# Kernel optimization log

Hardware: AMD Instinct MI355X
Metric: run time of the kernel (lower is better)

Reference implementation:

```python
import jax, jax.numpy as jnp
import numpy as np

S, B, L, V, D, T, G = 16, 8, 8, 32000, 1024, 512, 3


def setup_inputs() -> dict:
    key = jax.random.key(0)
    k = jax.random.split(key, 10)
    s = 0.05
    return {
        "encoded_hidden": jax.random.normal(k[0], (B, D), jnp.float32),
        "encoded_outputs": jax.random.normal(k[1], (B, T, D), jnp.float32),
        "story": jax.random.randint(k[2], (B, T), 0, V),
        "trg_batches": jax.random.randint(k[3], (B, S, L), 0, V),
        "embedding": jax.random.normal(k[4], (V, D), jnp.float32) * 0.1,
        "w_ih": jax.random.normal(k[5], (3 * D, D), jnp.float32) * s,
        "w_hh": jax.random.normal(k[6], (3 * D, D), jnp.float32) * s,
        "b_ih": jnp.zeros((3 * D,), jnp.float32),
        "b_hh": jnp.zeros((3 * D,), jnp.float32),
        "w_ratio_w": jax.random.normal(k[7], (1, 3 * D), jnp.float32) * s,
        "w_ratio_b": jnp.zeros((1,), jnp.float32),
        "w_gate_w": jax.random.normal(k[8], (G, D), jnp.float32) * s,
        "w_gate_b": jnp.zeros((G,), jnp.float32),
        "slot_emb": jax.random.normal(k[9], (S, D), jnp.float32) * 0.1,
    }


def reference(encoded_hidden, encoded_outputs, story, trg_batches, embedding,
              w_ih, w_hh, b_ih, b_hh, w_ratio_w, w_ratio_b,
              w_gate_w, w_gate_b, slot_emb):
    # Decoder inputs per (slot, step): step 0 = slot embedding,
    # step i>0 = embedding of teacher-forced target token i-1.  -> x: (S,L,B,D)
    x0 = jnp.broadcast_to(slot_emb[:, None, None, :], (S, 1, B, D))
    xt = jnp.transpose(embedding[trg_batches[:, :, :L - 1]], (1, 2, 0, 3))  # (S,L-1,B,D)
    x = jnp.concatenate([x0, xt], axis=1)

    # Single GRU step; hidden is reset to the encoder hidden each step (as in source),
    # so decoder_state == new hidden and all (slot,step) cells are independent.
    h0 = encoded_hidden  # (B,D)
    gi = jnp.einsum('slbd,ed->slbe', x, w_ih) + b_ih          # (S,L,B,3D)
    gh = h0 @ w_hh.T + b_hh                                    # (B,3D)
    ir, iz, inn = jnp.split(gi, 3, axis=-1)
    hr, hz, hn = jnp.split(gh, 3, axis=-1)
    r = jax.nn.sigmoid(ir + hr)
    z = jax.nn.sigmoid(iz + hz)
    n = jnp.tanh(inn + r * hn)
    h = (1.0 - z) * n + z * h0                                 # (S,L,B,D)

    # History attention; NOTE: context uses the RAW scores (source quirk).
    scores = jnp.einsum('slbd,btd->slbt', h, encoded_outputs)  # (S,L,B,T)
    probs = jax.nn.softmax(scores, axis=-1)
    context = jnp.einsum('slbt,btd->slbd', scores, encoded_outputs)

    # Vocab distribution p_vocab = softmax(h @ E^T)
    p_vocab = jax.nn.softmax(jnp.einsum('slbd,vd->slbv', h, embedding), axis=-1)

    # Pointer-generator gate
    feat = jnp.concatenate([h, context, x], axis=-1)           # (S,L,B,3D)
    p_gen = jax.nn.sigmoid(jnp.einsum('slbe,oe->slbo', feat, w_ratio_w) + w_ratio_b)  # (S,L,B,1)

    # Copy distribution via scatter-add of attention probs onto vocab ids
    def scatter_one(p_b, story_b):  # p_b: (S,L,T), story_b: (T,)
        return jnp.zeros((S, L, V), p_b.dtype).at[:, :, story_b].add(p_b)
    p_ctx = jax.vmap(scatter_one, in_axes=(2, 0), out_axes=2)(probs, story)  # (S,L,B,V)

    p_final = p_gen * p_vocab + (1.0 - p_gen) * p_ctx
    ptr_outputs = jnp.transpose(p_final, (0, 2, 1, 3))         # (S,B,L,V)
    gate_outputs = context[:, 0] @ w_gate_w.T + w_gate_b       # (S,B,G), from step 0
    return ptr_outputs, gate_outputs
```

## Files before the change

### kernel.cpp

```cpp
#include <hip/hip_runtime.h>

#define S_ 16
#define B_ 8
#define L_ 8
#define V_ 32000
#define D_ 1024
#define T_ 512
#define G_ 3
#define M_ 1024
#define E3_ 3072
#define NT_ 250

typedef unsigned short U16;
typedef __attribute__((ext_vector_type(8))) short short8;
typedef __attribute__((ext_vector_type(4))) float f32x4;

__device__ __forceinline__ U16 f2bf(float f) {
  union { float f; unsigned u; } c; c.f = f;
  unsigned u = c.u;
  return (U16)((u + 0x7FFFu + ((u >> 16) & 1u)) >> 16);
}
__device__ __forceinline__ float bf2f(U16 h) {
  union { unsigned u; float f; } c; c.u = ((unsigned)h) << 16;
  return c.f;
}
__device__ __forceinline__ void split2(float f, U16& hi, U16& lo) {
  hi = f2bf(f);
  lo = f2bf(f - bf2f(hi));
}

__global__ void k_cast_emb(const float* __restrict__ emb, U16* __restrict__ emb_bf) {
  int idx = blockIdx.x * 256 + threadIdx.x;
  float4 v = ((const float4*)emb)[idx];
  ushort4 o;
  o.x = f2bf(v.x); o.y = f2bf(v.y); o.z = f2bf(v.z); o.w = f2bf(v.w);
  ((ushort4*)emb_bf)[idx] = o;
}

__global__ void k_cast_wih(const float* __restrict__ w, U16* __restrict__ wh, U16* __restrict__ wl) {
  int idx = blockIdx.x * 256 + threadIdx.x;
  float4 v = ((const float4*)w)[idx];
  ushort4 h4, l4;
  split2(v.x, h4.x, l4.x); split2(v.y, h4.y, l4.y);
  split2(v.z, h4.z, l4.z); split2(v.w, h4.w, l4.w);
  ((ushort4*)wh)[idx] = h4;
  ((ushort4*)wl)[idx] = l4;
}

__global__ void k_cast_enc(const float* __restrict__ enc,
                           U16* __restrict__ enc_h, U16* __restrict__ enc_l,
                           U16* __restrict__ encT_h, U16* __restrict__ encT_l) {
  __shared__ U16 hs[32][36];
  __shared__ U16 ls[32][36];
  int b = blockIdx.z, t0 = blockIdx.x * 32, d0 = blockIdx.y * 32;
  int r  = threadIdx.x >> 3;
  int c4 = (threadIdx.x & 7) * 4;
  size_t src_idx = ((size_t)(b * T_ + t0 + r)) * D_ + d0 + c4;
  float4 v = *(const float4*)(enc + src_idx);
  ushort4 h4, l4;
  split2(v.x, h4.x, l4.x); split2(v.y, h4.y, l4.y);
  split2(v.z, h4.z, l4.z); split2(v.w, h4.w, l4.w);
  *(ushort4*)(enc_h + src_idx) = h4;
  *(ushort4*)(enc_l + src_idx) = l4;
  hs[r][c4+0] = h4.x; hs[r][c4+1] = h4.y; hs[r][c4+2] = h4.z; hs[r][c4+3] = h4.w;
  ls[r][c4+0] = l4.x; ls[r][c4+1] = l4.y; ls[r][c4+2] = l4.z; ls[r][c4+3] = l4.w;
  __syncthreads();
  ushort4 th, tl;
  th.x = hs[c4+0][r]; th.y = hs[c4+1][r]; th.z = hs[c4+2][r]; th.w = hs[c4+3][r];
  tl.x = ls[c4+0][r]; tl.y = ls[c4+1][r]; tl.z = ls[c4+2][r]; tl.w = ls[c4+3][r];
  size_t dst_idx = ((size_t)(b * D_ + d0 + r)) * T_ + t0 + c4;
  *(ushort4*)(encT_h + dst_idx) = th;
  *(ushort4*)(encT_l + dst_idx) = tl;
}

__global__ void k_build_x(const float* __restrict__ emb, const float* __restrict__ slot_emb,
                          const int* __restrict__ trg, float* __restrict__ x,
                          U16* __restrict__ x_h, U16* __restrict__ x_l) {
  int m = blockIdx.x;
  int d = threadIdx.x * 4;
  int b = m >> 7, s = (m >> 3) & 15, l = m & 7;
  const float* src;
  if (l == 0) src = slot_emb + s * D_;
  else        src = emb + (size_t)trg[b * (S_ * L_) + s * L_ + (l - 1)] * D_;
  float4 v = *(const float4*)(src + d);
  *(float4*)(x + (size_t)m * D_ + d) = v;
  ushort4 h4, l4;
  split2(v.x, h4.x, l4.x); split2(v.y, h4.y, l4.y);
  split2(v.z, h4.z, l4.z); split2(v.w, h4.w, l4.w);
  *(ushort4*)(x_h + (size_t)m * D_ + d) = h4;
  *(ushort4*)(x_l + (size_t)m * D_ + d) = l4;
}

__global__ void k_gh(const float* __restrict__ h0, const float* __restrict__ w_hh,
                     const float* __restrict__ b_hh, float* __restrict__ gh) {
  int b = blockIdx.y;
  int e = blockIdx.x * 64 + (threadIdx.x >> 2);
  int part = threadIdx.x & 3;
  const float* hr = h0 + b * D_ + part * 256;
  const float* wr = w_hh + (size_t)e * D_ + part * 256;
  float s = 0.f;
  for (int i = 0; i < 256; ++i) s += hr[i] * wr[i];
  s += __shfl_xor(s, 1);
  s += __shfl_xor(s, 2);
  if (part == 0) gh[b * E3_ + e] = s + b_hh[e];
}

template <int BK>
__device__ __forceinline__ void stage_tile(U16* __restrict__ sm, const U16* __restrict__ g,
                                           int row0, int k0, int lda, int tid) {
  constexpr int PASSES = (128 * BK * 2) / 4096;
#pragma unroll
  for (int i = 0; i < PASSES; ++i) {
    int o = (i * 256 + tid) * 16;
    int row, gc;
    if constexpr (BK == 32) {
      row = o >> 6;
      gc = ((o >> 4) & 3) ^ ((row >> 1) & 3);
    } else {
      row = o >> 7;
      gc = ((o >> 4) & 7) ^ (row & 7);
    }
    const U16* gp = g + (size_t)(row0 + row) * lda + k0 + gc * 8;
    U16* sp = sm + (o >> 1);
    __builtin_amdgcn_global_load_lds((const __attribute__((address_space(1))) unsigned int*)gp,
                                     (__attribute__((address_space(3))) unsigned int*)sp,
                                     16, 0, 0);
  }
}

template <int BK>
__device__ __forceinline__ short8 frag_ld(const U16* __restrict__ sm, int rowbase, int ln, int kh) {
  int row = rowbase + (ln & 15);
  if constexpr (BK == 32) {
    int c = (ln >> 4) ^ ((row >> 1) & 3);
    return *(const short8*)(sm + row * 32 + c * 8);
  } else {
    int c = (kh * 4 + (ln >> 4)) ^ (row & 7);
    return *(const short8*)(sm + row * 64 + c * 8);
  }
}

template <int BK, bool HILO, bool VOCAB, bool SWAP>
__global__ __launch_bounds__(256, 2)
void k_gemm(const U16* __restrict__ Ah, const U16* __restrict__ Al,
            const U16* __restrict__ Bh, const U16* __restrict__ Bl,
            float* __restrict__ C, float* __restrict__ part,
            int Ktot, int lda, int ldb, int ldc,
            long sA, long sB, long sC) {
  constexpr int TILE_U16 = 128 * BK;
  __shared__ U16 smem[(HILO ? 4 : 2) * TILE_U16];
  __shared__ float rsred[128];
  U16* Ash = smem;
  U16* Bsh = smem + TILE_U16;
  U16* Asl = HILO ? (smem + 2 * TILE_U16) : smem;
  U16* Bsl = HILO ? (smem + 3 * TILE_U16) : smem;

  int tid = threadIdx.x;
  int ln = tid & 63, w = tid >> 6;
  int wr = (w >> 1) * 64, wc = (w & 1) * 64;
  int m0 = (SWAP ? blockIdx.x : blockIdx.y) * 128;
  int n0 = (SWAP ? blockIdx.y : blockIdx.x) * 128;
  int ntile = SWAP ? blockIdx.y : blockIdx.x;
  int bz = blockIdx.z;
  const U16* pAh = Ah + (size_t)bz * sA;
  const U16* pBh = Bh + (size_t)bz * sB;
  const U16* pAl = HILO ? (Al + (size_t)bz * sA) : nullptr;
  const U16* pBl = HILO ? (Bl + (size_t)bz * sB) : nullptr;

  if constexpr (VOCAB) {
    if (tid < 128) rsred[tid] = 0.f;
  }

  f32x4 acc[4][4];
#pragma unroll
  for (int i = 0; i < 4; i++)
#pragma unroll
    for (int j = 0; j < 4; j++) acc[i][j] = (f32x4)(0.f);

  for (int k0 = 0; k0 < Ktot; k0 += BK) {
    __syncthreads();
    stage_tile<BK>(Ash, pAh, m0, k0, lda, tid);
    stage_tile<BK>(Bsh, pBh, n0, k0, ldb, tid);
    if constexpr (HILO) {
      stage_tile<BK>(Asl, pAl, m0, k0, lda, tid);
      stage_tile<BK>(Bsl, pBl, n0, k0, ldb, tid);
    }
    __syncthreads();

#pragma unroll
    for (int kh = 0; kh < BK / 32; kh++) {
      short8 a_h[4], b_h[4];
#pragma unroll
      for (int i = 0; i < 4; i++) {
        a_h[i] = frag_ld<BK>(Ash, wr + i * 16, ln, kh);
        b_h[i] = frag_ld<BK>(Bsh, wc + i * 16, ln, kh);
      }
      if constexpr (HILO) {
        short8 a_l[4], b_l[4];
#pragma unroll
        for (int i = 0; i < 4; i++) {
          a_l[i] = frag_ld<BK>(Asl, wr + i * 16, ln, kh);
          b_l[i] = frag_ld<BK>(Bsl, wc + i * 16, ln, kh);
        }
#pragma unroll
        for (int i = 0; i < 4; i++)
#pragma unroll
          for (int j = 0; j < 4; j++) {
            acc[i][j] = __builtin_amdgcn_mfma_f32_16x16x32_bf16(a_h[i], b_h[j], acc[i][j], 0, 0, 0);
            acc[i][j] = __builtin_amdgcn_mfma_f32_16x16x32_bf16(a_h[i], b_l[j], acc[i][j], 0, 0, 0);
            acc[i][j] = __builtin_amdgcn_mfma_f32_16x16x32_bf16(a_l[i], b_h[j], acc[i][j], 0, 0, 0);
          }
      } else {
#pragma unroll
        for (int i = 0; i < 4; i++)
#pragma unroll
          for (int j = 0; j < 4; j++)
            acc[i][j] = __builtin_amdgcn_mfma_f32_16x16x32_bf16(a_h[i], b_h[j], acc[i][j], 0, 0, 0);
      }
    }
  }

  int quad = ln >> 4, col = ln & 15;
  if constexpr (!VOCAB) {
    float* pC = C + (size_t)bz * sC;
#pragma unroll
    for (int i = 0; i < 4; i++)
#pragma unroll
      for (int j = 0; j < 4; j++)
#pragma unroll
        for (int r = 0; r < 4; r++)
          pC[(size_t)(m0 + wr + i * 16 + quad * 4 + r) * ldc + (n0 + wc + j * 16 + col)] =
              acc[i][j][r];
  } else {
#pragma unroll
    for (int i = 0; i < 4; i++)
#pragma unroll
      for (int r = 0; r < 4; r++) {
        int m = m0 + wr + i * 16 + quad * 4 + r;
        int s_ = (m >> 3) & 15, l_ = m & 7, b_ = m >> 7;
        size_t obase = (size_t)((s_ * B_ + b_) * L_ + l_) * (size_t)V_;
        float rs = 0.f;
#pragma unroll
        for (int j = 0; j < 4; j++) {
          float e = __expf(acc[i][j][r]);
          C[obase + (n0 + wc + j * 16 + col)] = e;
          rs += e;
        }
        rs += __shfl_xor(rs, 1);
        rs += __shfl_xor(rs, 2);
        rs += __shfl_xor(rs, 4);
        rs += __shfl_xor(rs, 8);
        if (col == 0) atomicAdd(&rsred[(wr + i * 16 + quad * 4 + r)], rs);
      }
    __syncthreads();
    if (tid < 128) part[(size_t)ntile * M_ + (m0 + tid)] = rsred[tid];
  }
}

__global__ void k_h(const float* __restrict__ gi, const float* __restrict__ gh,
                    const float* __restrict__ h0, const float* __restrict__ b_ih,
                    float* __restrict__ h, U16* __restrict__ h_h, U16* __restrict__ h_l) {
  int m = blockIdx.x;
  int d = threadIdx.x * 4;
  int b = m >> 7;
  float4 ir  = *(const float4*)(gi + (size_t)m * E3_ + d);
  float4 iz  = *(const float4*)(gi + (size_t)m * E3_ + D_ + d);
  float4 in_ = *(const float4*)(gi + (size_t)m * E3_ + 2 * D_ + d);
  float4 bir = *(const float4*)(b_ih + d);
  float4 biz = *(const float4*)(b_ih + D_ + d);
  float4 bin = *(const float4*)(b_ih + 2 * D_ + d);
  float4 hr  = *(const float4*)(gh + b * E3_ + d);
  float4 hz  = *(const float4*)(gh + b * E3_ + D_ + d);
  float4 hn  = *(const float4*)(gh + b * E3_ + 2 * D_ + d);
  float4 h0v = *(const float4*)(h0 + b * D_ + d);
  float4 out;
#define GRU1(c)                                             \
  {                                                         \
    float rr = 1.f / (1.f + __expf(-(ir.c + bir.c + hr.c))); \
    float zz = 1.f / (1.f + __expf(-(iz.c + biz.c + hz.c))); \
    float nn = tanhf(in_.c + bin.c + rr * hn.c);            \
    out.c = (1.f - zz) * nn + zz * h0v.c;                   \
  }
  GRU1(x) GRU1(y) GRU1(z) GRU1(w)
#undef GRU1
  *(float4*)(h + (size_t)m * D_ + d) = out;
  ushort4 h4, l4;
  split2(out.x, h4.x, l4.x); split2(out.y, h4.y, l4.y);
  split2(out.z, h4.z, l4.z); split2(out.w, h4.w, l4.w);
  *(ushort4*)(h_h + (size_t)m * D_ + d) = h4;
  *(ushort4*)(h_l + (size_t)m * D_ + d) = l4;
}

__global__ void k_softmax(const float* __restrict__ scores, float* __restrict__ probs,
                          U16* __restrict__ s_h, U16* __restrict__ s_l) {
  int m = blockIdx.x;
  int tid = threadIdx.x;
  int ln = tid & 63, w = tid >> 6;
  float v0 = scores[(size_t)m * T_ + tid];
  float v1 = scores[(size_t)m * T_ + 256 + tid];
  U16 hh, ll;
  split2(v0, hh, ll); s_h[m * T_ + tid] = hh;       s_l[m * T_ + tid] = ll;
  split2(v1, hh, ll); s_h[m * T_ + 256 + tid] = hh; s_l[m * T_ + 256 + tid] = ll;
  float mx = fmaxf(v0, v1);
#pragma unroll
  for (int msk = 32; msk >= 1; msk >>= 1) mx = fmaxf(mx, __shfl_xor(mx, msk));
  __shared__ float red[4];
  if (ln == 0) red[w] = mx;
  __syncthreads();
  mx = fmaxf(fmaxf(red[0], red[1]), fmaxf(red[2], red[3]));
  float e0 = __expf(v0 - mx), e1 = __expf(v1 - mx);
  float sm = e0 + e1;
#pragma unroll
  for (int msk = 32; msk >= 1; msk >>= 1) sm += __shfl_xor(sm, msk);
  __syncthreads();
  if (ln == 0) red[w] = sm;
  __syncthreads();
  float inv = 1.f / (red[0] + red[1] + red[2] + red[3]);
  probs[(size_t)m * T_ + tid] = e0 * inv;
  probs[(size_t)m * T_ + 256 + tid] = e1 * inv;
}

__global__ void k_pgen(const float* __restrict__ h, const float* __restrict__ ctx,
                       const float* __restrict__ x, const float* __restrict__ wr,
                       const float* __restrict__ wrb, float* __restrict__ p_gen) {
  int m = blockIdx.x;
  int tid = threadIdx.x;
  int ln = tid & 63, w = tid >> 6;
  float sacc = 0.f;
  for (int j = tid; j < D_; j += 256)
    sacc += h[(size_t)m * D_ + j] * wr[j] + ctx[(size_t)m * D_ + j] * wr[D_ + j] +
            x[(size_t)m * D_ + j] * wr[2 * D_ + j];
#pragma unroll
  for (int msk = 32; msk >= 1; msk >>= 1) sacc += __shfl_xor(sacc, msk);
  __shared__ float red[4];
  if (ln == 0) red[w] = sacc;
  __syncthreads();
  if (tid == 0) {
    float t = red[0] + red[1] + red[2] + red[3] + wrb[0];
    p_gen[m] = 1.f / (1.f + expf(-t));
  }
}

__global__ void k_gate(const float* __restrict__ ctx, const float* __restrict__ wg,
                       const float* __restrict__ wgb, float* __restrict__ out_gate) {
  int id = blockIdx.x;
  int g = id % 3;
  int sb = id / 3;
  int b = sb & 7, s = sb >> 3;
  int m = (b * S_ + s) * L_;
  int ln = threadIdx.x;
  float acc = 0.f;
  for (int d = ln; d < D_; d += 64) acc += ctx[(size_t)m * D_ + d] * wg[g * D_ + d];
#pragma unroll
  for (int msk = 32; msk >= 1; msk >>= 1) acc += __shfl_xor(acc, msk);
  if (ln == 0) out_gate[id] = acc + wgb[g];
}

__global__ void k_scale(float* __restrict__ out, const float* __restrict__ p_gen,
                        const float* __restrict__ part) {
  int m = blockIdx.x;
  int tid = threadIdx.x, ln = tid & 63, w = tid >> 6;
  float ps = (tid < NT_) ? part[(size_t)tid * M_ + m] : 0.f;
#pragma unroll
  for (int msk = 32; msk >= 1; msk >>= 1) ps += __shfl_xor(ps, msk);
  __shared__ float red[4];
  __shared__ float scs;
  if (ln == 0) red[w] = ps;
  __syncthreads();
  if (tid == 0) scs = p_gen[m] / (red[0] + red[1] + red[2] + red[3]);
  __syncthreads();
  float sc = scs;
  int b = m >> 7, s = (m >> 3) & 15, l = m & 7;
  float4* p = (float4*)(out + (size_t)((s * B_ + b) * L_ + l) * (size_t)V_);
  for (int j = tid; j < V_ / 4; j += 256) {
    float4 v = p[j];
    v.x *= sc; v.y *= sc; v.z *= sc; v.w *= sc;
    p[j] = v;
  }
}

__global__ void k_scatter(float* __restrict__ out, const float* __restrict__ p_gen,
                          const float* __restrict__ probs, const int* __restrict__ story) {
  int id = blockIdx.x * 256 + threadIdx.x;
  int m = id >> 9, t = id & 511;
  int b = m >> 7, s = (m >> 3) & 15, l = m & 7;
  float val = (1.f - p_gen[m]) * probs[(size_t)m * T_ + t];
  int v = story[b * T_ + t];
  size_t o = (size_t)((s * B_ + b) * L_ + l) * (size_t)V_ + v;
  atomicAdd(out + o, val);
}

extern "C" void kernel_launch(void* const* d_in, const int* in_sizes, int n_in,
                              void* d_out, int out_size, void* d_ws, size_t ws_size,
                              hipStream_t stream) {
  (void)in_sizes; (void)n_in; (void)out_size; (void)ws_size;
  const float* enc_hid   = (const float*)d_in[0];
  const float* enc_out   = (const float*)d_in[1];
  const int*   story     = (const int*)d_in[2];
  const int*   trg       = (const int*)d_in[3];
  const float* emb       = (const float*)d_in[4];
  const float* w_ih      = (const float*)d_in[5];
  const float* w_hh      = (const float*)d_in[6];
  const float* b_ih      = (const float*)d_in[7];
  const float* b_hh      = (const float*)d_in[8];
  const float* w_ratio_w = (const float*)d_in[9];
  const float* w_ratio_b = (const float*)d_in[10];
  const float* w_gate_w  = (const float*)d_in[11];
  const float* w_gate_b  = (const float*)d_in[12];
  const float* slot_emb  = (const float*)d_in[13];
  float* out = (float*)d_out;

  char* ws = (char*)d_ws;
  size_t off = 0;
  auto alloc = [&](size_t bytes) -> void* {
    void* p = ws + off;
    off += (bytes + 255) & ~(size_t)255;
    return p;
  };
  U16* emb_bf   = (U16*)alloc((size_t)V_ * D_ * 2);
  float* x      = (float*)alloc((size_t)M_ * D_ * 4);
  U16* x_h      = (U16*)alloc((size_t)M_ * D_ * 2);
  U16* x_l      = (U16*)alloc((size_t)M_ * D_ * 2);
  U16* wih_h    = (U16*)alloc((size_t)E3_ * D_ * 2);
  U16* wih_l    = (U16*)alloc((size_t)E3_ * D_ * 2);
  U16* enc_h    = (U16*)alloc((size_t)B_ * T_ * D_ * 2);
  U16* enc_l    = (U16*)alloc((size_t)B_ * T_ * D_ * 2);
  U16* encT_h   = (U16*)alloc((size_t)B_ * T_ * D_ * 2);
  U16* encT_l   = (U16*)alloc((size_t)B_ * T_ * D_ * 2);
  float* gh     = (float*)alloc((size_t)B_ * E3_ * 4);
  float* gi     = (float*)alloc((size_t)M_ * E3_ * 4);
  float* h      = (float*)alloc((size_t)M_ * D_ * 4);
  U16* h_h      = (U16*)alloc((size_t)M_ * D_ * 2);
  U16* h_l      = (U16*)alloc((size_t)M_ * D_ * 2);
  float* scores = (float*)alloc((size_t)M_ * T_ * 4);
  U16* sc_h     = (U16*)alloc((size_t)M_ * T_ * 2);
  U16* sc_l     = (U16*)alloc((size_t)M_ * T_ * 2);
  float* probs  = (float*)alloc((size_t)M_ * T_ * 4);
  float* ctx    = (float*)alloc((size_t)M_ * D_ * 4);
  float* p_gen  = (float*)alloc((size_t)M_ * 4);
  float* part   = (float*)alloc((size_t)NT_ * M_ * 4);

  k_cast_emb<<<V_ * D_ / 4 / 256, 256, 0, stream>>>(emb, emb_bf);
  k_cast_wih<<<E3_ * D_ / 4 / 256, 256, 0, stream>>>(w_ih, wih_h, wih_l);
  k_cast_enc<<<dim3(T_ / 32, D_ / 32, B_), 256, 0, stream>>>(enc_out, enc_h, enc_l, encT_h, encT_l);
  k_build_x<<<M_, 256, 0, stream>>>(emb, slot_emb, trg, x, x_h, x_l);
  k_gh<<<dim3(E3_ / 64, B_), 256, 0, stream>>>(enc_hid, w_hh, b_hh, gh);

  k_gemm<32, true, false, false><<<dim3(E3_ / 128, M_ / 128, 1), 256, 0, stream>>>(
      x_h, x_l, wih_h, wih_l, gi, nullptr, D_, D_, D_, E3_, 0, 0, 0);

  k_h<<<M_, 256, 0, stream>>>(gi, gh, enc_hid, b_ih, h, h_h, h_l);

  k_gemm<32, true, false, false><<<dim3(T_ / 128, 1, B_), 256, 0, stream>>>(
      h_h, h_l, enc_h, enc_l, scores, nullptr, D_, D_, D_, T_,
      (long)(S_ * L_) * D_, (long)T_ * D_, (long)(S_ * L_) * T_);

  k_softmax<<<M_, 256, 0, stream>>>(scores, probs, sc_h, sc_l);

  k_gemm<32, true, false, false><<<dim3(D_ / 128, 1, B_), 256, 0, stream>>>(
      sc_h, sc_l, encT_h, encT_l, ctx, nullptr, T_, T_, T_, D_,
      (long)(S_ * L_) * T_, (long)D_ * T_, (long)(S_ * L_) * D_);

  k_pgen<<<M_, 256, 0, stream>>>(h, ctx, x, w_ratio_w, w_ratio_b, p_gen);
  k_gate<<<S_ * B_ * G_, 64, 0, stream>>>(ctx, w_gate_w, w_gate_b, out + (size_t)M_ * V_);

  k_gemm<64, false, true, true><<<dim3(M_ / 128, V_ / 128, 1), 256, 0, stream>>>(
      h_h, nullptr, emb_bf, nullptr, out, part, D_, D_, D_, V_, 0, 0, 0);

  k_scale<<<M_, 256, 0, stream>>>(out, p_gen, part);
  k_scatter<<<M_ * T_ / 256, 256, 0, stream>>>(out, p_gen, probs, story);
}
```

Baseline: 593.7 us.

## Replace attention GEMMs with fp32 SIMT kernels, fuse scatter, remap vocab grid

The encoder cast/transpose kernel and the hi/lo split bf16 MFMA GEMMs for scores and context are replaced by direct fp32 SIMT kernels that read encoded_outputs and stage h or scores in LDS. This removes the conversion passes and their extra buffers. The scatter is fused into k_scale as per-row atomics after scaling. The vocab GEMM uses a 1D grid with a remapped tile order, and the GRU input GEMM moves to BK=64. The h low-part buffer is dropped since only the vocab GEMM uses the bf16 hidden state. The fp32 SIMT attention kernels have far lower peak throughput than MFMA, which is the main risk.

```diff
diff --git a/kernel.cpp b/kernel.cpp
--- a/kernel.cpp
+++ b/kernel.cpp
@@ -45,32 +45,6 @@
   split2(v.z, h4.z, l4.z); split2(v.w, h4.w, l4.w);
   ((ushort4*)wh)[idx] = h4;
   ((ushort4*)wl)[idx] = l4;
-}
-
-__global__ void k_cast_enc(const float* __restrict__ enc,
-                           U16* __restrict__ enc_h, U16* __restrict__ enc_l,
-                           U16* __restrict__ encT_h, U16* __restrict__ encT_l) {
-  __shared__ U16 hs[32][36];
-  __shared__ U16 ls[32][36];
-  int b = blockIdx.z, t0 = blockIdx.x * 32, d0 = blockIdx.y * 32;
-  int r  = threadIdx.x >> 3;
-  int c4 = (threadIdx.x & 7) * 4;
-  size_t src_idx = ((size_t)(b * T_ + t0 + r)) * D_ + d0 + c4;
-  float4 v = *(const float4*)(enc + src_idx);
-  ushort4 h4, l4;
-  split2(v.x, h4.x, l4.x); split2(v.y, h4.y, l4.y);
-  split2(v.z, h4.z, l4.z); split2(v.w, h4.w, l4.w);
-  *(ushort4*)(enc_h + src_idx) = h4;
-  *(ushort4*)(enc_l + src_idx) = l4;
-  hs[r][c4+0] = h4.x; hs[r][c4+1] = h4.y; hs[r][c4+2] = h4.z; hs[r][c4+3] = h4.w;
-  ls[r][c4+0] = l4.x; ls[r][c4+1] = l4.y; ls[r][c4+2] = l4.z; ls[r][c4+3] = l4.w;
-  __syncthreads();
-  ushort4 th, tl;
-  th.x = hs[c4+0][r]; th.y = hs[c4+1][r]; th.z = hs[c4+2][r]; th.w = hs[c4+3][r];
-  tl.x = ls[c4+0][r]; tl.y = ls[c4+1][r]; tl.z = ls[c4+2][r]; tl.w = ls[c4+3][r];
-  size_t dst_idx = ((size_t)(b * D_ + d0 + r)) * T_ + t0 + c4;
-  *(ushort4*)(encT_h + dst_idx) = th;
-  *(ushort4*)(encT_l + dst_idx) = tl;
 }
 
 __global__ void k_build_x(const float* __restrict__ emb, const float* __restrict__ slot_emb,
@@ -112,14 +86,8 @@
 #pragma unroll
   for (int i = 0; i < PASSES; ++i) {
     int o = (i * 256 + tid) * 16;
-    int row, gc;
-    if constexpr (BK == 32) {
-      row = o >> 6;
-      gc = ((o >> 4) & 3) ^ ((row >> 1) & 3);
-    } else {
-      row = o >> 7;
-      gc = ((o >> 4) & 7) ^ (row & 7);
-    }
+    int row = o >> 7;
+    int gc = ((o >> 4) & 7) ^ (row & 7);
     const U16* gp = g + (size_t)(row0 + row) * lda + k0 + gc * 8;
     U16* sp = sm + (o >> 1);
     __builtin_amdgcn_global_load_lds((const __attribute__((address_space(1))) unsigned int*)gp,
@@ -131,22 +99,16 @@
 template <int BK>
 __device__ __forceinline__ short8 frag_ld(const U16* __restrict__ sm, int rowbase, int ln, int kh) {
   int row = rowbase + (ln & 15);
-  if constexpr (BK == 32) {
-    int c = (ln >> 4) ^ ((row >> 1) & 3);
-    return *(const short8*)(sm + row * 32 + c * 8);
-  } else {
-    int c = (kh * 4 + (ln >> 4)) ^ (row & 7);
-    return *(const short8*)(sm + row * 64 + c * 8);
-  }
-}
-
-template <int BK, bool HILO, bool VOCAB, bool SWAP>
+  int c = (kh * 4 + (ln >> 4)) ^ (row & 7);
+  return *(const short8*)(sm + row * 64 + c * 8);
+}
+
+template <int BK, bool HILO, bool VOCAB>
 __global__ __launch_bounds__(256, 2)
 void k_gemm(const U16* __restrict__ Ah, const U16* __restrict__ Al,
             const U16* __restrict__ Bh, const U16* __restrict__ Bl,
             float* __restrict__ C, float* __restrict__ part,
-            int Ktot, int lda, int ldb, int ldc,
-            long sA, long sB, long sC) {
+            int Ktot, int lda, int ldb, int ldc) {
   constexpr int TILE_U16 = 128 * BK;
   __shared__ U16 smem[(HILO ? 4 : 2) * TILE_U16];
   __shared__ float rsred[128];
@@ -158,14 +120,17 @@
   int tid = threadIdx.x;
   int ln = tid & 63, w = tid >> 6;
   int wr = (w >> 1) * 64, wc = (w & 1) * 64;
-  int m0 = (SWAP ? blockIdx.x : blockIdx.y) * 128;
-  int n0 = (SWAP ? blockIdx.y : blockIdx.x) * 128;
-  int ntile = SWAP ? blockIdx.y : blockIdx.x;
-  int bz = blockIdx.z;
-  const U16* pAh = Ah + (size_t)bz * sA;
-  const U16* pBh = Bh + (size_t)bz * sB;
-  const U16* pAl = HILO ? (Al + (size_t)bz * sA) : nullptr;
-  const U16* pBl = HILO ? (Bl + (size_t)bz * sB) : nullptr;
+  int m0, n0, ntile = 0;
+  if constexpr (VOCAB) {
+    int bid = blockIdx.x;
+    int tile = (bid & 7) * NT_ + (bid >> 3);
+    ntile = tile >> 3;
+    m0 = (tile & 7) * 128;
+    n0 = ntile * 128;
+  } else {
+    m0 = blockIdx.y * 128;
+    n0 = blockIdx.x * 128;
+  }
 
   if constexpr (VOCAB) {
     if (tid < 128) rsred[tid] = 0.f;
@@ -179,11 +144,11 @@
 
   for (int k0 = 0; k0 < Ktot; k0 += BK) {
     __syncthreads();
-    stage_tile<BK>(Ash, pAh, m0, k0, lda, tid);
-    stage_tile<BK>(Bsh, pBh, n0, k0, ldb, tid);
+    stage_tile<BK>(Ash, Ah, m0, k0, lda, tid);
+    stage_tile<BK>(Bsh, Bh, n0, k0, ldb, tid);
     if constexpr (HILO) {
-      stage_tile<BK>(Asl, pAl, m0, k0, lda, tid);
-      stage_tile<BK>(Bsl, pBl, n0, k0, ldb, tid);
+      stage_tile<BK>(Asl, Al, m0, k0, lda, tid);
+      stage_tile<BK>(Bsl, Bl, n0, k0, ldb, tid);
     }
     __syncthreads();
 
@@ -222,14 +187,13 @@
 
   int quad = ln >> 4, col = ln & 15;
   if constexpr (!VOCAB) {
-    float* pC = C + (size_t)bz * sC;
 #pragma unroll
     for (int i = 0; i < 4; i++)
 #pragma unroll
       for (int j = 0; j < 4; j++)
 #pragma unroll
         for (int r = 0; r < 4; r++)
-          pC[(size_t)(m0 + wr + i * 16 + quad * 4 + r) * ldc + (n0 + wc + j * 16 + col)] =
+          C[(size_t)(m0 + wr + i * 16 + quad * 4 + r) * ldc + (n0 + wc + j * 16 + col)] =
               acc[i][j][r];
   } else {
 #pragma unroll
@@ -259,7 +223,7 @@
 
 __global__ void k_h(const float* __restrict__ gi, const float* __restrict__ gh,
                     const float* __restrict__ h0, const float* __restrict__ b_ih,
-                    float* __restrict__ h, U16* __restrict__ h_h, U16* __restrict__ h_l) {
+                    float* __restrict__ h, U16* __restrict__ h_h) {
   int m = blockIdx.x;
   int d = threadIdx.x * 4;
   int b = m >> 7;
@@ -284,23 +248,80 @@
   GRU1(x) GRU1(y) GRU1(z) GRU1(w)
 #undef GRU1
   *(float4*)(h + (size_t)m * D_ + d) = out;
-  ushort4 h4, l4;
-  split2(out.x, h4.x, l4.x); split2(out.y, h4.y, l4.y);
-  split2(out.z, h4.z, l4.z); split2(out.w, h4.w, l4.w);
+  ushort4 h4;
+  h4.x = f2bf(out.x); h4.y = f2bf(out.y); h4.z = f2bf(out.z); h4.w = f2bf(out.w);
   *(ushort4*)(h_h + (size_t)m * D_ + d) = h4;
-  *(ushort4*)(h_l + (size_t)m * D_ + d) = l4;
-}
-
-__global__ void k_softmax(const float* __restrict__ scores, float* __restrict__ probs,
-                          U16* __restrict__ s_h, U16* __restrict__ s_l) {
+}
+
+__global__ void k_scores(const float* __restrict__ h, const float* __restrict__ enc,
+                         float* __restrict__ scores) {
+  __shared__ float hs[8 * D_];
+  int t0 = blockIdx.x * 128, mc = blockIdx.y, b = blockIdx.z;
+  int tid = threadIdx.x;
+  int mbase = b * 128 + mc * 8;
+  const float4* hsrc = (const float4*)(h + (size_t)mbase * D_);
+  float4* hs4 = (float4*)hs;
+  for (int i = tid; i < 8 * D_ / 4; i += 256) hs4[i] = hsrc[i];
+  __syncthreads();
+  int j = tid & 127, rg = (tid >> 7) * 4;
+  const float4* e4 = (const float4*)(enc + ((size_t)b * T_ + t0 + j) * D_);
+  const float4* h0p = (const float4*)(hs + (rg + 0) * D_);
+  const float4* h1p = (const float4*)(hs + (rg + 1) * D_);
+  const float4* h2p = (const float4*)(hs + (rg + 2) * D_);
+  const float4* h3p = (const float4*)(hs + (rg + 3) * D_);
+  float a0 = 0.f, a1 = 0.f, a2 = 0.f, a3 = 0.f;
+#pragma unroll 4
+  for (int k = 0; k < D_ / 4; k++) {
+    float4 e = e4[k];
+    float4 v0 = h0p[k], v1 = h1p[k], v2 = h2p[k], v3 = h3p[k];
+    a0 += e.x * v0.x + e.y * v0.y + e.z * v0.z + e.w * v0.w;
+    a1 += e.x * v1.x + e.y * v1.y + e.z * v1.z + e.w * v1.w;
+    a2 += e.x * v2.x + e.y * v2.y + e.z * v2.z + e.w * v2.w;
+    a3 += e.x * v3.x + e.y * v3.y + e.z * v3.z + e.w * v3.w;
+  }
+  scores[(size_t)(mbase + rg + 0) * T_ + t0 + j] = a0;
+  scores[(size_t)(mbase + rg + 1) * T_ + t0 + j] = a1;
+  scores[(size_t)(mbase + rg + 2) * T_ + t0 + j] = a2;
+  scores[(size_t)(mbase + rg + 3) * T_ + t0 + j] = a3;
+}
+
+__global__ void k_ctx(const float* __restrict__ scores, const float* __restrict__ enc,
+                      float* __restrict__ ctx) {
+  __shared__ float ss[8 * T_];
+  int d0 = blockIdx.x * 128, mc = blockIdx.y, b = blockIdx.z;
+  int tid = threadIdx.x;
+  int mbase = b * 128 + mc * 8;
+  const float4* ssrc = (const float4*)(scores + (size_t)mbase * T_);
+  float4* ss4 = (float4*)ss;
+  for (int i = tid; i < 8 * T_ / 4; i += 256) ss4[i] = ssrc[i];
+  __syncthreads();
+  int j = tid & 127, rg = (tid >> 7) * 4;
+  int d = d0 + j;
+  const float* s0 = ss + (rg + 0) * T_;
+  const float* s1 = ss + (rg + 1) * T_;
+  const float* s2 = ss + (rg + 2) * T_;
+  const float* s3 = ss + (rg + 3) * T_;
+  float a0 = 0.f, a1 = 0.f, a2 = 0.f, a3 = 0.f;
+#pragma unroll 8
+  for (int t = 0; t < T_; t++) {
+    float e = enc[((size_t)b * T_ + t) * D_ + d];
+    a0 += e * s0[t];
+    a1 += e * s1[t];
+    a2 += e * s2[t];
+    a3 += e * s3[t];
+  }
+  ctx[(size_t)(mbase + rg + 0) * D_ + d] = a0;
+  ctx[(size_t)(mbase + rg + 1) * D_ + d] = a1;
+  ctx[(size_t)(mbase + rg + 2) * D_ + d] = a2;
+  ctx[(size_t)(mbase + rg + 3) * D_ + d] = a3;
+}
+
+__global__ void k_softmax(const float* __restrict__ scores, float* __restrict__ probs) {
   int m = blockIdx.x;
   int tid = threadIdx.x;
   int ln = tid & 63, w = tid >> 6;
   float v0 = scores[(size_t)m * T_ + tid];
   float v1 = scores[(size_t)m * T_ + 256 + tid];
-  U16 hh, ll;
-  split2(v0, hh, ll); s_h[m * T_ + tid] = hh;       s_l[m * T_ + tid] = ll;
-  split2(v1, hh, ll); s_h[m * T_ + 256 + tid] = hh; s_l[m * T_ + 256 + tid] = ll;
   float mx = fmaxf(v0, v1);
 #pragma unroll
   for (int msk = 32; msk >= 1; msk >>= 1) mx = fmaxf(mx, __shfl_xor(mx, msk));
@@ -357,7 +378,8 @@
 }
 
 __global__ void k_scale(float* __restrict__ out, const float* __restrict__ p_gen,
-                        const float* __restrict__ part) {
+                        const float* __restrict__ part, const float* __restrict__ probs,
+                        const int* __restrict__ story) {
   int m = blockIdx.x;
   int tid = threadIdx.x, ln = tid & 63, w = tid >> 6;
   float ps = (tid < NT_) ? part[(size_t)tid * M_ + m] : 0.f;
@@ -371,23 +393,17 @@
   __syncthreads();
   float sc = scs;
   int b = m >> 7, s = (m >> 3) & 15, l = m & 7;
-  float4* p = (float4*)(out + (size_t)((s * B_ + b) * L_ + l) * (size_t)V_);
+  float* row = out + (size_t)((s * B_ + b) * L_ + l) * (size_t)V_;
+  float4* p = (float4*)row;
   for (int j = tid; j < V_ / 4; j += 256) {
     float4 v = p[j];
     v.x *= sc; v.y *= sc; v.z *= sc; v.w *= sc;
     p[j] = v;
   }
-}
-
-__global__ void k_scatter(float* __restrict__ out, const float* __restrict__ p_gen,
-                          const float* __restrict__ probs, const int* __restrict__ story) {
-  int id = blockIdx.x * 256 + threadIdx.x;
-  int m = id >> 9, t = id & 511;
-  int b = m >> 7, s = (m >> 3) & 15, l = m & 7;
-  float val = (1.f - p_gen[m]) * probs[(size_t)m * T_ + t];
-  int v = story[b * T_ + t];
-  size_t o = (size_t)((s * B_ + b) * L_ + l) * (size_t)V_ + v;
-  atomicAdd(out + o, val);
+  __syncthreads();
+  float om = 1.f - p_gen[m];
+  for (int t = tid; t < T_; t += 256)
+    atomicAdd(row + story[b * T_ + t], om * probs[(size_t)m * T_ + t]);
 }
 
 extern "C" void kernel_launch(void* const* d_in, const int* in_sizes, int n_in,
@@ -423,18 +439,11 @@
   U16* x_l      = (U16*)alloc((size_t)M_ * D_ * 2);
   U16* wih_h    = (U16*)alloc((size_t)E3_ * D_ * 2);
   U16* wih_l    = (U16*)alloc((size_t)E3_ * D_ * 2);
-  U16* enc_h    = (U16*)alloc((size_t)B_ * T_ * D_ * 2);
-  U16* enc_l    = (U16*)alloc((size_t)B_ * T_ * D_ * 2);
-  U16* encT_h   = (U16*)alloc((size_t)B_ * T_ * D_ * 2);
-  U16* encT_l   = (U16*)alloc((size_t)B_ * T_ * D_ * 2);
   float* gh     = (float*)alloc((size_t)B_ * E3_ * 4);
   float* gi     = (float*)alloc((size_t)M_ * E3_ * 4);
   float* h      = (float*)alloc((size_t)M_ * D_ * 4);
   U16* h_h      = (U16*)alloc((size_t)M_ * D_ * 2);
-  U16* h_l      = (U16*)alloc((size_t)M_ * D_ * 2);
   float* scores = (float*)alloc((size_t)M_ * T_ * 4);
-  U16* sc_h     = (U16*)alloc((size_t)M_ * T_ * 2);
-  U16* sc_l     = (U16*)alloc((size_t)M_ * T_ * 2);
   float* probs  = (float*)alloc((size_t)M_ * T_ * 4);
   float* ctx    = (float*)alloc((size_t)M_ * D_ * 4);
   float* p_gen  = (float*)alloc((size_t)M_ * 4);
@@ -442,31 +451,25 @@
 
   k_cast_emb<<<V_ * D_ / 4 / 256, 256, 0, stream>>>(emb, emb_bf);
   k_cast_wih<<<E3_ * D_ / 4 / 256, 256, 0, stream>>>(w_ih, wih_h, wih_l);
-  k_cast_enc<<<dim3(T_ / 32, D_ / 32, B_), 256, 0, stream>>>(enc_out, enc_h, enc_l, encT_h, encT_l);
   k_build_x<<<M_, 256, 0, stream>>>(emb, slot_emb, trg, x, x_h, x_l);
   k_gh<<<dim3(E3_ / 64, B_), 256, 0, stream>>>(enc_hid, w_hh, b_hh, gh);
 
-  k_gemm<32, true, false, false><<<dim3(E3_ / 128, M_ / 128, 1), 256, 0, stream>>>(
-      x_h, x_l, wih_h, wih_l, gi, nullptr, D_, D_, D_, E3_, 0, 0, 0);
-
-  k_h<<<M_, 256, 0, stream>>>(gi, gh, enc_hid, b_ih, h, h_h, h_l);
-
-  k_gemm<32, true, false, false><<<dim3(T_ / 128, 1, B_), 256, 0, stream>>>(
-      h_h, h_l, enc_h, enc_l, scores, nullptr, D_, D_, D_, T_,
-      (long)(S_ * L_) * D_, (long)T_ * D_, (long)(S_ * L_) * T_);
-
-  k_softmax<<<M_, 256, 0, stream>>>(scores, probs, sc_h, sc_l);
-
-  k_gemm<32, true, false, false><<<dim3(D_ / 128, 1, B_), 256, 0, stream>>>(
-      sc_h, sc_l, encT_h, encT_l, ctx, nullptr, T_, T_, T_, D_,
-      (long)(S_ * L_) * T_, (long)D_ * T_, (long)(S_ * L_) * D_);
+  k_gemm<64, true, false><<<dim3(E3_ / 128, M_ / 128), 256, 0, stream>>>(
+      x_h, x_l, wih_h, wih_l, gi, nullptr, D_, D_, D_, E3_);
+
+  k_h<<<M_, 256, 0, stream>>>(gi, gh, enc_hid, b_ih, h, h_h);
+
+  k_scores<<<dim3(4, 16, 8), 256, 0, stream>>>(h, enc_out, scores);
+
+  k_softmax<<<M_, 256, 0, stream>>>(scores, probs);
+
+  k_ctx<<<dim3(8, 16, 8), 256, 0, stream>>>(scores, enc_out, ctx);
 
   k_pgen<<<M_, 256, 0, stream>>>(h, ctx, x, w_ratio_w, w_ratio_b, p_gen);
   k_gate<<<S_ * B_ * G_, 64, 0, stream>>>(ctx, w_gate_w, w_gate_b, out + (size_t)M_ * V_);
 
-  k_gemm<64, false, true, true><<<dim3(M_ / 128, V_ / 128, 1), 256, 0, stream>>>(
-      h_h, nullptr, emb_bf, nullptr, out, part, D_, D_, D_, V_, 0, 0, 0);
-
-  k_scale<<<M_, 256, 0, stream>>>(out, p_gen, part);
-  k_scatter<<<M_ * T_ / 256, 256, 0, stream>>>(out, p_gen, probs, story);
-}
+  k_gemm<64, false, true><<<dim3(8 * NT_), 256, 0, stream>>>(
+      h_h, nullptr, emb_bf, nullptr, out, part, D_, D_, D_, V_);
+
+  k_scale<<<M_, 256, 0, stream>>>(out, p_gen, part, probs, story);
+}
```

New measurement: 585.6 us. Within noise of the previous version (-1.4%).
